# Kernel tuning notes

Hardware: AMD Instinct MI355X
Metric: run time of the kernel (lower is better)

Reference implementation:

```python
import jax, jax.numpy as jnp
import numpy as np

B, S, D, H, FF = 2, 2048, 1024, 16, 4096
HD = D // H          # head dim = 64
ROT = HD // 2        # rotary dim = dim/(num_heads*2) = 32 (partial rotation)
EPS = 1e-5


def setup_inputs() -> dict:
    key = jax.random.key(0)
    ks = jax.random.split(key, 16)
    std = 0.02
    return {
        "x": jax.random.normal(ks[0], (B, S, D), jnp.float32),
        "mask": jnp.ones((B, 1, 1, S), jnp.int32),
        "wq": jax.random.normal(ks[1], (D, D), jnp.float32) * std,
        "bq": jnp.zeros((D,), jnp.float32),
        "wk": jax.random.normal(ks[2], (D, D), jnp.float32) * std,
        "bk": jnp.zeros((D,), jnp.float32),
        "wv": jax.random.normal(ks[3], (D, D), jnp.float32) * std,
        "bv": jnp.zeros((D,), jnp.float32),
        "wo": jax.random.normal(ks[4], (D, D), jnp.float32) * std,
        "bo": jnp.zeros((D,), jnp.float32),
        "ln1_w": jnp.ones((D,), jnp.float32),
        "ln1_b": jnp.zeros((D,), jnp.float32),
        "ln2_w": jnp.ones((D,), jnp.float32),
        "ln2_b": jnp.zeros((D,), jnp.float32),
        "w1": jax.random.normal(ks[5], (D, FF), jnp.float32) * std,
        "b1": jnp.zeros((FF,), jnp.float32),
        "w2": jax.random.normal(ks[6], (FF, D), jnp.float32) * std,
        "b2": jnp.zeros((D,), jnp.float32),
    }


def _layernorm(x, w, b):
    mu = jnp.mean(x, axis=-1, keepdims=True)
    var = jnp.mean(jnp.square(x - mu), axis=-1, keepdims=True)
    return (x - mu) * jax.lax.rsqrt(var + EPS) * w + b


def _rope(t):
    # t: [B, H, S, HD]; rotate first ROT features, interleaved (GPT-J) pairing
    inv_freq = 1.0 / (10000.0 ** (jnp.arange(0, ROT, 2, dtype=jnp.float32) / ROT))
    ang = jnp.arange(S, dtype=jnp.float32)[:, None] * inv_freq      # [S, ROT//2]
    ang = jnp.repeat(ang, 2, axis=-1)                               # [S, ROT]
    cos, sin = jnp.cos(ang), jnp.sin(ang)
    t_rot, t_pass = t[..., :ROT], t[..., ROT:]
    pr = t_rot.reshape(*t_rot.shape[:-1], ROT // 2, 2)
    rot = jnp.stack([-pr[..., 1], pr[..., 0]], axis=-1).reshape(t_rot.shape)
    return jnp.concatenate([t_rot * cos + rot * sin, t_pass], axis=-1)


def reference(x, mask, wq, bq, wk, bk, wv, bv, wo, bo,
              ln1_w, ln1_b, ln2_w, ln2_b, w1, b1, w2, b2):
    res = x
    h = _layernorm(x, ln1_w, ln1_b)
    q = (h @ wq + bq).reshape(B, S, H, HD).transpose(0, 2, 1, 3)
    k = (h @ wk + bk).reshape(B, S, H, HD).transpose(0, 2, 1, 3)
    v = (h @ wv + bv).reshape(B, S, H, HD).transpose(0, 2, 1, 3)
    q, k = _rope(q), _rope(k)
    score = jnp.einsum('bhqd,bhkd->bhqk', q, k) * (1.0 / np.sqrt(HD))
    score = jnp.where(mask == 0, jnp.float32(-1e9), score)
    attn = jax.nn.softmax(score, axis=-1)
    out = jnp.einsum('bhqk,bhkd->bhqd', attn, v)
    out = out.transpose(0, 2, 1, 3).reshape(B, S, D) @ wo + bo
    x = res + out
    res = x
    h = _layernorm(x, ln2_w, ln2_b)
    h = jax.nn.gelu(h @ w1 + b1, approximate=False) @ w2 + b2
    return res + h
```

## Files before the change

### kernel.cpp

```cpp
#include <hip/hip_runtime.h>
#include <cstdint>
#include <cstddef>


typedef __bf16 bf16;
typedef __bf16 bf16x2 __attribute__((ext_vector_type(2)));
typedef __bf16 bf16x4v __attribute__((ext_vector_type(4)));
typedef __bf16 bf16x8 __attribute__((ext_vector_type(8)));
typedef float  f32x4  __attribute__((ext_vector_type(4)));

#define NB 2
#define NS 2048
#define ND 1024
#define NH 16
#define NHD 64
#define NFF 4096
#define NM (NB*NS)
#define QKSCALE 0.18033688011112042f

typedef uint32_t __attribute__((address_space(1))) gu32_t;
typedef uint32_t __attribute__((address_space(3))) lu32_t;
__device__ __forceinline__ void async_copy16(void* lds, const void* g) {
  __builtin_amdgcn_global_load_lds((gu32_t*)g, (lu32_t*)lds, 16, 0, 0);
}

__device__ __forceinline__ float gelu_f(float x) {
  return 0.5f * x * (1.0f + erff(x * 0.70710678118654752f));
}

__global__ __launch_bounds__(256) void prep_kernel(
    const float* __restrict__ wq, const float* __restrict__ wk,
    const float* __restrict__ wv, const float* __restrict__ wo,
    const float* __restrict__ w1, const float* __restrict__ w2,
    bf16* __restrict__ wqt, bf16* __restrict__ wkt, bf16* __restrict__ wvt,
    bf16* __restrict__ wot, bf16* __restrict__ w1t, bf16* __restrict__ w2t,
    const float* __restrict__ bq, const float* __restrict__ bk,
    const float* __restrict__ bv, float* __restrict__ bcat,
    const int* __restrict__ mask, float* __restrict__ m01f,
    bf16* __restrict__ m01b, float2* __restrict__ rtab,
    const float* __restrict__ x, const float* __restrict__ ln1w,
    const float* __restrict__ ln1b, bf16* __restrict__ h1) {
  int flat = blockIdx.x;
  int t = threadIdx.x;
  if (flat < 12288) {
    __shared__ float tile[32][33];
    const float* W; bf16* Wt; long bx, by; int K, N;
    if (flat < 4096) {
      int which = flat >> 10, r = flat & 1023;
      const float* Ws[4] = {wq, wk, wv, wo};
      bf16* Wts[4] = {wqt, wkt, wvt, wot};
      W = Ws[which]; Wt = Wts[which]; bx = r & 31; by = r >> 5; K = ND; N = ND;
    } else if (flat < 8192) {
      int r = flat - 4096;
      W = w1; Wt = w1t; bx = r & 127; by = r >> 7; K = ND; N = NFF;
    } else {
      int r = flat - 8192;
      W = w2; Wt = w2t; bx = r & 31; by = r >> 5; K = NFF; N = ND;
    }
    int tx = t & 31, ty = t >> 5;
#pragma unroll
    for (int r = 0; r < 4; ++r)
      tile[ty + r*8][tx] = W[(by*32 + ty + r*8) * (long)N + bx*32 + tx];
    __syncthreads();
#pragma unroll
    for (int r = 0; r < 4; ++r)
      Wt[(bx*32 + ty + r*8) * (long)K + by*32 + tx] = (bf16)tile[tx][ty + r*8];
  } else if (flat < 12444) {
    int blk = flat - 12288;
    if (blk < 12) {
      int i = blk * 256 + t;
      bcat[i] = (i < ND) ? bq[i] : ((i < 2*ND) ? bk[i - ND] : bv[i - 2*ND]);
    } else if (blk < 28) {
      int i = (blk - 12) * 256 + t;
      float v = mask[i] ? 1.0f : 0.0f;
      m01f[i] = v;
      m01b[i] = (bf16)v;
    } else {
      int idx = (blk - 28) * 256 + t;
      int s = idx >> 4, i = idx & 15;
      float ang = (float)s * exp2f(-(float)i * (13.287712379549449f / 16.0f));
      float sn, cs;
      sincosf(ang, &sn, &cs);
      rtab[idx] = make_float2(cs, sn);
    }
  } else {
    long row = flat - 12444;
    float4 v = ((const float4*)(x + row*ND))[t];
    float s  = v.x + v.y + v.z + v.w;
    float sq = v.x*v.x + v.y*v.y + v.z*v.z + v.w*v.w;
#pragma unroll
    for (int m = 1; m <= 32; m <<= 1) { s += __shfl_xor(s, m); sq += __shfl_xor(sq, m); }
    __shared__ float ss[4], ssq[4];
    if ((t & 63) == 0) { ss[t>>6] = s; ssq[t>>6] = sq; }
    __syncthreads();
    s  = ss[0] + ss[1] + ss[2] + ss[3];
    sq = ssq[0] + ssq[1] + ssq[2] + ssq[3];
    float mu = s * (1.0f/ND);
    float rs = rsqrtf(sq * (1.0f/ND) - mu*mu + 1e-5f);
    float4 wv4 = ((const float4*)ln1w)[t];
    float4 bv4 = ((const float4*)ln1b)[t];
    bf16x4v o;
    o[0] = (bf16)((v.x-mu)*rs*wv4.x + bv4.x);
    o[1] = (bf16)((v.y-mu)*rs*wv4.y + bv4.y);
    o[2] = (bf16)((v.z-mu)*rs*wv4.z + bv4.z);
    o[3] = (bf16)((v.w-mu)*rs*wv4.w + bv4.w);
    *(bf16x4v*)(h1 + row*ND + t*4) = o;
  }
}

__global__ __launch_bounds__(256) void vtrans_kernel(
    const bf16* __restrict__ v, bf16* __restrict__ vt) {
  __shared__ bf16 t[64][66];
  int st = blockIdx.x, bh = blockIdx.y;
  int b = bh >> 4, h = bh & 15;
  int c = threadIdx.x & 63, rg = threadIdx.x >> 6;
  const bf16* src = v + ((long)b*NS + st*64)*ND + h*64;
#pragma unroll
  for (int i = 0; i < 16; ++i) {
    int r = rg*16 + i;
    t[r][c] = src[(long)r*ND + c];
  }
  __syncthreads();
  bf16* dst = vt + (long)bh*64*NS + st*64;
#pragma unroll
  for (int i = 0; i < 16; ++i) {
    int d = rg*16 + i;
    dst[(long)d*NS + c] = t[c][d];
  }
}

__global__ __launch_bounds__(256) void ln_kernel(
    const float* __restrict__ x, const float* __restrict__ w,
    const float* __restrict__ b, bf16* __restrict__ out) {
  long row = blockIdx.x;
  int t = threadIdx.x;
  float4 v = ((const float4*)(x + row*ND))[t];
  float s  = v.x + v.y + v.z + v.w;
  float sq = v.x*v.x + v.y*v.y + v.z*v.z + v.w*v.w;
#pragma unroll
  for (int m = 1; m <= 32; m <<= 1) { s += __shfl_xor(s, m); sq += __shfl_xor(sq, m); }
  __shared__ float ss[4], ssq[4];
  if ((t & 63) == 0) { ss[t>>6] = s; ssq[t>>6] = sq; }
  __syncthreads();
  s  = ss[0] + ss[1] + ss[2] + ss[3];
  sq = ssq[0] + ssq[1] + ssq[2] + ssq[3];
  float mu = s * (1.0f/ND);
  float rs = rsqrtf(sq * (1.0f/ND) - mu*mu + 1e-5f);
  float4 wv = ((const float4*)w)[t];
  float4 bv = ((const float4*)b)[t];
  bf16x4v o;
  o[0] = (bf16)((v.x-mu)*rs*wv.x + bv.x);
  o[1] = (bf16)((v.y-mu)*rs*wv.y + bv.y);
  o[2] = (bf16)((v.z-mu)*rs*wv.z + bv.z);
  o[3] = (bf16)((v.w-mu)*rs*wv.w + bv.w);
  *(bf16x4v*)(out + row*ND + t*4) = o;
}

__global__ __launch_bounds__(256) void ffn2red_kernel(
    const bf16* __restrict__ P, const float* __restrict__ y1,
    const float* __restrict__ b2, float* __restrict__ out) {
  const long n8 = (long)NM * ND / 8;
  for (long i = (long)blockIdx.x*256 + threadIdx.x; i < n8;
       i += (long)gridDim.x*256) {
    bf16x8 p0 = ((const bf16x8*)P)[i];
    bf16x8 p1 = ((const bf16x8*)P)[i + n8];
    bf16x8 p2 = ((const bf16x8*)P)[i + 2*n8];
    bf16x8 p3 = ((const bf16x8*)P)[i + 3*n8];
    float4 ya = ((const float4*)y1)[2*i];
    float4 yb = ((const float4*)y1)[2*i + 1];
    int cb = (int)((i * 8) & 1023);
    float4 ba = *(const float4*)&b2[cb];
    float4 bb = *(const float4*)&b2[cb + 4];
    float4 ra, rb;
    ra.x = ((float)p0[0]+(float)p1[0])+((float)p2[0]+(float)p3[0]) + ya.x + ba.x;
    ra.y = ((float)p0[1]+(float)p1[1])+((float)p2[1]+(float)p3[1]) + ya.y + ba.y;
    ra.z = ((float)p0[2]+(float)p1[2])+((float)p2[2]+(float)p3[2]) + ya.z + ba.z;
    ra.w = ((float)p0[3]+(float)p1[3])+((float)p2[3]+(float)p3[3]) + ya.w + ba.w;
    rb.x = ((float)p0[4]+(float)p1[4])+((float)p2[4]+(float)p3[4]) + yb.x + bb.x;
    rb.y = ((float)p0[5]+(float)p1[5])+((float)p2[5]+(float)p3[5]) + yb.y + bb.y;
    rb.z = ((float)p0[6]+(float)p1[6])+((float)p2[6]+(float)p3[6]) + yb.z + bb.z;
    rb.w = ((float)p0[7]+(float)p1[7])+((float)p2[7]+(float)p3[7]) + yb.w + bb.w;
    ((float4*)out)[2*i]     = ra;
    ((float4*)out)[2*i + 1] = rb;
  }
}

template<int EPI>
__global__ __launch_bounds__(512, 2) void gemm256_kernel(
    const bf16* __restrict__ A, const bf16* __restrict__ Bt,
    const float* __restrict__ bias, void* __restrict__ Cout,
    const float2* __restrict__ rtab, const float* __restrict__ m01f,
    int M, int N, int K, int lda, int ldbt) {
  __shared__ __align__(16) bf16 Alds[2][256*64];
  __shared__ __align__(16) bf16 Blds[2][256*64];
  const int tid = threadIdx.x, lane = tid & 63, w = tid >> 6;
  const int fr = lane & 15, kg = lane >> 4;
  const int wr = w >> 2, wc = w & 3;
  const int kz = (EPI == 2) ? blockIdx.z : 0;
  const long kofs = (long)kz * K;

  const int gx = gridDim.x;
  int lin = blockIdx.y * gx + blockIdx.x;
  int nwg = gx * gridDim.y;
  int swz = (lin & 7) * (nwg >> 3) + (lin >> 3);
  const long am0 = (long)(swz / gx) * 256;
  const long bn0 = (long)(swz % gx) * 256;

  const f32x4 fzero = {0.f, 0.f, 0.f, 0.f};
  f32x4 acc[8][4];
#pragma unroll
  for (int m = 0; m < 8; ++m)
#pragma unroll
    for (int n = 0; n < 4; ++n) acc[m][n] = fzero;

  auto stage = [&](int kt, int bufi) {
#pragma unroll
    for (int i = 0; i < 4; ++i) {
      int s = i*512 + tid;
      int r = s >> 3, c = (s & 7) ^ (r & 7);
      async_copy16((char*)&Alds[bufi][0] + i*8192 + w*1024,
                   &A[(am0 + r)*(long)lda + kofs + kt + c*8]);
    }
#pragma unroll
    for (int i = 0; i < 4; ++i) {
      int s = i*512 + tid;
      int r = s >> 3, c = (s & 7) ^ (r & 7);
      async_copy16((char*)&Blds[bufi][0] + i*8192 + w*1024,
                   &Bt[(bn0 + r)*(long)ldbt + kofs + kt + c*8]);
    }
  };

  const int nk = K >> 6;
  stage(0, 0);
  stage(64, 1);
  asm volatile("s_waitcnt vmcnt(8)" ::: "memory");
  __builtin_amdgcn_s_barrier();
  __builtin_amdgcn_sched_barrier(0);

  for (int t = 0; t < nk; ++t) {
    const char* Ab = (const char*)&Alds[t & 1][0];
    const char* Bb = (const char*)&Blds[t & 1][0];
    bf16x8 bfv0[4], bfv1[4], af[4];
#pragma unroll
    for (int n = 0; n < 4; ++n) {
      int r = wc*64 + n*16 + fr;
      bfv0[n] = *(const bf16x8*)(Bb + r*128 + ((kg ^ (r & 7)) << 4));
    }
#pragma unroll
    for (int m = 0; m < 4; ++m) {
      int r = wr*128 + m*16 + fr;
      af[m] = *(const bf16x8*)(Ab + r*128 + ((kg ^ (r & 7)) << 4));
    }
    asm volatile("s_waitcnt lgkmcnt(0)" ::: "memory");
    __builtin_amdgcn_sched_barrier(0);
    __builtin_amdgcn_s_setprio(1);
#pragma unroll
    for (int m = 0; m < 4; ++m)
#pragma unroll
      for (int n = 0; n < 4; ++n)
        acc[m][n] = __builtin_amdgcn_mfma_f32_16x16x32_bf16(af[m], bfv0[n], acc[m][n], 0, 0, 0);
    __builtin_amdgcn_s_setprio(0);
#pragma unroll
    for (int n = 0; n < 4; ++n) {
      int r = wc*64 + n*16 + fr;
      bfv1[n] = *(const bf16x8*)(Bb + r*128 + (((4 + kg) ^ (r & 7)) << 4));
    }
#pragma unroll
    for (int m = 0; m < 4; ++m) {
      int r = wr*128 + m*16 + fr;
      af[m] = *(const bf16x8*)(Ab + r*128 + (((4 + kg) ^ (r & 7)) << 4));
    }
    asm volatile("s_waitcnt lgkmcnt(0)" ::: "memory");
    __builtin_amdgcn_sched_barrier(0);
    __builtin_amdgcn_s_setprio(1);
#pragma unroll
    for (int m = 0; m < 4; ++m)
#pragma unroll
      for (int n = 0; n < 4; ++n)
        acc[m][n] = __builtin_amdgcn_mfma_f32_16x16x32_bf16(af[m], bfv1[n], acc[m][n], 0, 0, 0);
    __builtin_amdgcn_s_setprio(0);
#pragma unroll
    for (int m = 0; m < 4; ++m) {
      int r = wr*128 + (m+4)*16 + fr;
      af[m] = *(const bf16x8*)(Ab + r*128 + ((kg ^ (r & 7)) << 4));
    }
    asm volatile("s_waitcnt lgkmcnt(0)" ::: "memory");
    __builtin_amdgcn_sched_barrier(0);
    __builtin_amdgcn_s_setprio(1);
#pragma unroll
    for (int m = 0; m < 4; ++m)
#pragma unroll
      for (int n = 0; n < 4; ++n)
        acc[m+4][n] = __builtin_amdgcn_mfma_f32_16x16x32_bf16(af[m], bfv0[n], acc[m+4][n], 0, 0, 0);
    __builtin_amdgcn_s_setprio(0);
#pragma unroll
    for (int m = 0; m < 4; ++m) {
      int r = wr*128 + (m+4)*16 + fr;
      af[m] = *(const bf16x8*)(Ab + r*128 + (((4 + kg) ^ (r & 7)) << 4));
    }
    asm volatile("s_waitcnt lgkmcnt(0)" ::: "memory");
    __builtin_amdgcn_sched_barrier(0);
    __builtin_amdgcn_s_setprio(1);
#pragma unroll
    for (int m = 0; m < 4; ++m)
#pragma unroll
      for (int n = 0; n < 4; ++n)
        acc[m+4][n] = __builtin_amdgcn_mfma_f32_16x16x32_bf16(af[m], bfv1[n], acc[m+4][n], 0, 0, 0);
    __builtin_amdgcn_s_setprio(0);

    if (t + 1 == nk) break;
    __builtin_amdgcn_s_barrier();
    __builtin_amdgcn_sched_barrier(0);
    if (t + 2 < nk) {
      stage((t + 2) * 64, t & 1);
      asm volatile("s_waitcnt vmcnt(8)" ::: "memory");
    } else {
      asm volatile("s_waitcnt vmcnt(0)" ::: "memory");
    }
    __builtin_amdgcn_s_barrier();
    __builtin_amdgcn_sched_barrier(0);
  }

  const int rbase = kg * 4;
  const int region = (int)(bn0 >> 10);
#pragma unroll
  for (int m = 0; m < 8; ++m) {
#pragma unroll
    for (int n = 0; n < 4; ++n) {
      long col = bn0 + wc*64 + n*16 + fr;
      float bia = (EPI == 2) ? 0.0f : bias[col];
#pragma unroll
      for (int j = 0; j < 4; ++j) {
        long row = am0 + wr*128 + m*16 + rbase + j;
        float val = acc[m][n][j] + bia;
        if (EPI == 1) {
          ((bf16*)Cout)[row * N + col] = (bf16)gelu_f(val);
        } else if (EPI == 2) {
          ((bf16*)Cout)[((long)kz * NM + row) * N + col] = (bf16)val;
        } else {
          long cv = col & 1023;
          if (region <= 1) {
            float pval = __shfl_xor(val, 1);
            if (n < 2) {
              float2 cs = rtab[((row & (NS-1)) << 4) | ((n*16 + fr) >> 1)];
              val = (fr & 1) ? val*cs.x + pval*cs.y : val*cs.x - pval*cs.y;
            }
            if (region == 0) val *= QKSCALE;
          } else {
            val *= m01f[row];
          }
          ((bf16*)Cout)[(long)region * (NM*(long)ND) + row * ND + cv] = (bf16)val;
        }
      }
    }
  }
}

__global__ __launch_bounds__(512, 1) void gemm128x8_kernel(
    const bf16* __restrict__ A, const bf16* __restrict__ Bt,
    const float* __restrict__ bias, const float* __restrict__ res,
    float* __restrict__ Cout, int M, int N, int K) {
  __shared__ __align__(16) bf16 Alds[4][128*64];
  __shared__ __align__(16) bf16 Blds[4][128*64];
  const int tid = threadIdx.x, lane = tid & 63, w = tid >> 6;
  const int fr = lane & 15, kg = lane >> 4;
  const int wr = w >> 1, wc = w & 1;

  const int gx = gridDim.x;
  int lin = blockIdx.y * gx + blockIdx.x;
  int nwg = gx * gridDim.y;
  int swz = (lin & 7) * (nwg >> 3) + (lin >> 3);
  const long am0 = (long)(swz / gx) * 128;
  const long bn0 = (long)(swz % gx) * 128;

  const f32x4 fzero = {0.f, 0.f, 0.f, 0.f};
  f32x4 acc[2][4];
#pragma unroll
  for (int m = 0; m < 2; ++m)
#pragma unroll
    for (int n = 0; n < 4; ++n) acc[m][n] = fzero;

  auto stage = [&](int kt, int bufi) {
#pragma unroll
    for (int i = 0; i < 2; ++i) {
      int s = i*512 + tid;
      int r = s >> 3, c = (s & 7) ^ (r & 7);
      async_copy16((char*)&Alds[bufi][0] + i*8192 + w*1024,
                   &A[(am0 + r)*K + kt + c*8]);
      async_copy16((char*)&Blds[bufi][0] + i*8192 + w*1024,
                   &Bt[(bn0 + r)*K + kt + c*8]);
    }
  };

  const int nk = K >> 6;
  stage(0, 0);
  stage(64, 1);
  asm volatile("s_waitcnt vmcnt(4)" ::: "memory");
  __builtin_amdgcn_s_barrier();
  __builtin_amdgcn_sched_barrier(0);

  for (int t = 0; t < nk; ++t) {
    const int cur = t & 3;
    if (t + 2 < nk) stage((t + 2) * 64, (t + 2) & 3);
    const char* Ab = (const char*)&Alds[cur][0];
    const char* Bb = (const char*)&Blds[cur][0];
    bf16x8 af[2][2], bfv[2][4];
#pragma unroll
    for (int kk = 0; kk < 2; ++kk) {
#pragma unroll
      for (int m = 0; m < 2; ++m) {
        int r = wr*32 + m*16 + fr;
        af[kk][m] = *(const bf16x8*)(Ab + r*128 + (((kk*4 + kg) ^ (r & 7)) << 4));
      }
#pragma unroll
      for (int n = 0; n < 4; ++n) {
        int r = wc*64 + n*16 + fr;
        bfv[kk][n] = *(const bf16x8*)(Bb + r*128 + (((kk*4 + kg) ^ (r & 7)) << 4));
      }
    }
    asm volatile("s_waitcnt lgkmcnt(0)" ::: "memory");
    __builtin_amdgcn_sched_barrier(0);
    __builtin_amdgcn_s_setprio(1);
#pragma unroll
    for (int kk = 0; kk < 2; ++kk)
#pragma unroll
      for (int m = 0; m < 2; ++m)
#pragma unroll
        for (int n = 0; n < 4; ++n)
          acc[m][n] = __builtin_amdgcn_mfma_f32_16x16x32_bf16(af[kk][m], bfv[kk][n], acc[m][n], 0, 0, 0);
    __builtin_amdgcn_s_setprio(0);
    if (t + 2 < nk) { asm volatile("s_waitcnt vmcnt(4)" ::: "memory"); }
    else            { asm volatile("s_waitcnt vmcnt(0)" ::: "memory"); }
    __builtin_amdgcn_s_barrier();
    __builtin_amdgcn_sched_barrier(0);
  }

  const int rbase = kg * 4;
#pragma unroll
  for (int m = 0; m < 2; ++m) {
#pragma unroll
    for (int n = 0; n < 4; ++n) {
      long col = bn0 + wc*64 + n*16 + fr;
      float bia = bias[col];
#pragma unroll
      for (int j = 0; j < 4; ++j) {
        long row = am0 + wr*32 + m*16 + rbase + j;
        Cout[row * N + col] = acc[m][n][j] + bia + res[row * N + col];
      }
    }
  }
}

__global__ __launch_bounds__(512, 4) void attn_kernel(
    const bf16* __restrict__ q, const bf16* __restrict__ k,
    const bf16* __restrict__ vt, const bf16* __restrict__ m01b,
    bf16* __restrict__ out) {
  int lin = blockIdx.y * 16 + blockIdx.x;
  int swz = (lin & 7) * 64 + (lin >> 3);
  const int qt = swz & 15;
  const int bh = swz >> 4;
  const int b = bh >> 4, h = bh & 15;
  const int tid = threadIdx.x, lane = tid & 63, w = tid >> 6;
  const int fr = lane & 15, kg = lane >> 4;
  const int k8 = kg * 8;
  const int frl = fr & 3, frh = fr >> 2;

  __shared__ __align__(16) bf16 KVlds[4][2][64*64];
  __shared__ __align__(16) bf16 Mlds[NS];

  const long qrow = (long)qt*128 + w*16 + fr;
  const bf16* qbase = q + ((long)b*NS + qrow)*ND + h*NHD;
  bf16x8 qf[2];
  qf[0] = *(const bf16x8*)(qbase + k8);
  qf[1] = *(const bf16x8*)(qbase + 32 + k8);

  const bf16* kbase = k + (long)b*NS*ND + h*NHD;
  const bf16* vtb = vt + (long)bh*64*NS;
  const bf16* mbase = m01b + (long)b*NS;

  if (w < 4) async_copy16((char*)Mlds + w*1024, mbase + tid*8);

  int aK[4][2], aV[2][4];
#pragma unroll
  for (int n = 0; n < 4; ++n) {
    int r = (frh << 3) + ((n & 1) << 2) + frl + ((n >> 1) << 5);
    int swzr = (r & 7) ^ (((r >> 3) & 1) << 2);
#pragma unroll
    for (int kk = 0; kk < 2; ++kk) {
      aK[n][kk] = r*128 + ((((kk << 2) | kg) ^ swzr) << 4);
      asm("" : "+v"(aK[n][kk]));
    }
  }
#pragma unroll
  for (int kk = 0; kk < 2; ++kk)
#pragma unroll
    for (int n2 = 0; n2 < 4; ++n2) {
      int r = n2*16 + fr;
      aV[kk][n2] = r*128 + ((((kk << 2) | kg) ^ (r & 7)) << 4);
      asm("" : "+v"(aV[kk][n2]));
    }

  const int srow = tid >> 3, sc = tid & 7;
  const int csK = (sc ^ (srow & 7) ^ (((srow >> 3) & 1) << 2));
  const int csV = (sc ^ (srow & 7));
  const bf16* kp = kbase + (long)srow*ND + csK*8;
  const bf16* vp = vtb + (long)srow*NS + csV*8;
  const int ldsoff = w*1024;

  const f32x4 fzero = {0.f, 0.f, 0.f, 0.f};
  f32x4 oacc[4], oaccL = fzero;
#pragma unroll
  for (int n = 0; n < 4; ++n) oacc[n] = fzero;

  async_copy16((char*)KVlds + 0*16384 + ldsoff, kp);
  async_copy16((char*)KVlds + 0*16384 + 8192 + ldsoff, vp);
  kp += 64*ND; vp += 64;
  async_copy16((char*)KVlds + 1*16384 + ldsoff, kp);
  async_copy16((char*)KVlds + 1*16384 + 8192 + ldsoff, vp);
  kp += 64*ND; vp += 64;
  asm volatile("s_waitcnt vmcnt(2)" ::: "memory");
  __builtin_amdgcn_s_barrier();
  __builtin_amdgcn_sched_barrier(0);

  const int NT = NS / 64;

#define ATTN_TILE(KT, BUF)                                                     \
  {                                                                            \
    const int kt_ = (KT);                                                      \
    if (kt_ + 2 < NT) {                                                        \
      async_copy16((char*)KVlds + (((BUF)+2)&3)*16384 + ldsoff, kp);           \
      async_copy16((char*)KVlds + (((BUF)+2)&3)*16384 + 8192 + ldsoff, vp);    \
      kp += 64*ND; vp += 64;                                                   \
    }                                                                          \
    bf16x8 vbm0 = *(const bf16x8*)&Mlds[kt_*64 + k8];                          \
    bf16x8 vbm1 = *(const bf16x8*)&Mlds[kt_*64 + 32 + k8];                     \
    f32x4 sacc[4];                                                             \
    _Pragma("unroll")                                                          \
    for (int n = 0; n < 4; ++n) sacc[n] = fzero;                               \
    _Pragma("unroll")                                                          \
    for (int n = 0; n < 4; ++n) {                                              \
      _Pragma("unroll")                                                        \
      for (int kk = 0; kk < 2; ++kk) {                                         \
        bf16x8 kf = *(const bf16x8*)((const char*)KVlds + (BUF)*16384 +        \
                                     aK[n][kk]);                               \
        sacc[n] = __builtin_amdgcn_mfma_f32_16x16x32_bf16(kf, qf[kk],          \
                                                          sacc[n], 0, 0, 0);   \
      }                                                                        \
    }                                                                          \
    float p[4][4];                                                             \
    _Pragma("unroll")                                                          \
    for (int n = 0; n < 4; ++n) {                                              \
      p[n][0] = exp2f(sacc[n][0]);                                             \
      p[n][1] = exp2f(sacc[n][1]);                                             \
      p[n][2] = exp2f(sacc[n][2]);                                             \
      p[n][3] = exp2f(sacc[n][3]);                                             \
    }                                                                          \
    bf16x8 paf[2];                                                             \
    _Pragma("unroll")                                                          \
    for (int n = 0; n < 4; ++n) {                                              \
      _Pragma("unroll")                                                        \
      for (int j = 0; j < 4; ++j)                                              \
        paf[n >> 1][((n & 1) << 2) + j] = (bf16)p[n][j];                       \
    }                                                                          \
    oaccL = __builtin_amdgcn_mfma_f32_16x16x32_bf16(paf[0], vbm0, oaccL,       \
                                                    0, 0, 0);                  \
    oaccL = __builtin_amdgcn_mfma_f32_16x16x32_bf16(paf[1], vbm1, oaccL,       \
                                                    0, 0, 0);                  \
    _Pragma("unroll")                                                          \
    for (int kk = 0; kk < 2; ++kk) {                                           \
      _Pragma("unroll")                                                        \
      for (int n2 = 0; n2 < 4; ++n2) {                                         \
        bf16x8 vb8 = *(const bf16x8*)((const char*)KVlds + (BUF)*16384 +       \
                                      8192 + aV[kk][n2]);                      \
        oacc[n2] = __builtin_amdgcn_mfma_f32_16x16x32_bf16(paf[kk], vb8,       \
                                                           oacc[n2], 0, 0, 0); \
      }                                                                        \
    }                                                                          \
    if (kt_ + 2 < NT)      { asm volatile("s_waitcnt vmcnt(2)" ::: "memory"); }\
    else if (kt_ + 1 < NT) { asm volatile("s_waitcnt vmcnt(0)" ::: "memory"); }\
    __builtin_amdgcn_s_barrier();                                              \
    __builtin_amdgcn_sched_barrier(0);                                         \
  }

  for (int it = 0; it < NT/4; ++it) {
    int kt0 = it * 4;
    ATTN_TILE(kt0 + 0, 0)
    ATTN_TILE(kt0 + 1, 1)
    ATTN_TILE(kt0 + 2, 2)
    ATTN_TILE(kt0 + 3, 3)
  }
#undef ATTN_TILE

#pragma unroll
  for (int j = 0; j < 4; ++j) {
    float inv = 1.0f / oaccL[j];
    long orow = (long)qt*128 + w*16 + kg*4 + j;
    bf16* ob = out + ((long)b*NS + orow)*ND + h*NHD;
#pragma unroll
    for (int n2 = 0; n2 < 4; ++n2) ob[n2*16 + fr] = (bf16)(oacc[n2][j] * inv);
  }
}

extern "C" void kernel_launch(void* const* d_in, const int* in_sizes, int n_in,
                              void* d_out, int out_size, void* d_ws, size_t ws_size,
                              hipStream_t stream) {
  const float* x    = (const float*)d_in[0];
  const int*   mask = (const int*)d_in[1];
  const float* wq   = (const float*)d_in[2];
  const float* bq   = (const float*)d_in[3];
  const float* wk   = (const float*)d_in[4];
  const float* bk   = (const float*)d_in[5];
  const float* wv   = (const float*)d_in[6];
  const float* bv   = (const float*)d_in[7];
  const float* wo   = (const float*)d_in[8];
  const float* bo   = (const float*)d_in[9];
  const float* ln1w = (const float*)d_in[10];
  const float* ln1b = (const float*)d_in[11];
  const float* ln2w = (const float*)d_in[12];
  const float* ln2b = (const float*)d_in[13];
  const float* w1   = (const float*)d_in[14];
  const float* b1   = (const float*)d_in[15];
  const float* w2   = (const float*)d_in[16];
  const float* b2   = (const float*)d_in[17];
  float* out = (float*)d_out;

  char* ws = (char*)d_ws;
  const size_t MB = 1024ull * 1024ull;
  bf16* wqt = (bf16*)(ws + 0*MB);
  bf16* wkt = (bf16*)(ws + 2*MB);
  bf16* wvt = (bf16*)(ws + 4*MB);
  bf16* wot = (bf16*)(ws + 6*MB);
  bf16* w1t = (bf16*)(ws + 8*MB);
  bf16* w2t = (bf16*)(ws + 16*MB);
  bf16* h1   = (bf16*)(ws + 24*MB);
  bf16* qb   = (bf16*)(ws + 32*MB);
  bf16* kb   = (bf16*)(ws + 40*MB);
  bf16* vb   = (bf16*)(ws + 48*MB);
  bf16* vtb  = h1;
  bf16* attnb = (bf16*)(ws + 72*MB);
  bf16* f1   = (bf16*)(ws + 24*MB);
  float* y1  = (float*)(ws + 56*MB);
  bf16* h2   = (bf16*)(ws + 72*MB);
  float* bcat = (float*)(ws + 80*MB);
  float* m01f = (float*)(ws + 80*MB + 16*1024);
  bf16*  m01b = (bf16*) (ws + 80*MB + 32*1024);
  float2* rtab = (float2*)(ws + 80*MB + 48*1024);
  bf16* pK   = (bf16*)(ws + 84*MB);
  const bool use_splitk = (ws_size >= 116ull*MB);
  (void)in_sizes; (void)n_in; (void)out_size;

  prep_kernel<<<16540, 256, 0, stream>>>(wq, wk, wv, wo, w1, w2,
                                         wqt, wkt, wvt, wot, w1t, w2t,
                                         bq, bk, bv, bcat, mask, m01f, m01b,
                                         rtab, x, ln1w, ln1b, h1);

  gemm256_kernel<3><<<dim3(12, 16), 512, 0, stream>>>(h1, wqt, bcat, qb,
                                                      rtab, m01f, NM, 3*ND, ND,
                                                      ND, ND);
  vtrans_kernel<<<dim3(32, 32), 256, 0, stream>>>(vb, vtb);

  attn_kernel<<<dim3(16, 32), 512, 0, stream>>>(qb, kb, vtb, m01b, attnb);

  gemm128x8_kernel<<<dim3(8, 32), 512, 0, stream>>>(attnb, wot, bo, x, y1,
                                                    NM, ND, ND);
  ln_kernel<<<NM, 256, 0, stream>>>(y1, ln2w, ln2b, h2);
  gemm256_kernel<1><<<dim3(16, 16), 512, 0, stream>>>(h2, w1t, b1, f1,
                                                      nullptr, nullptr,
                                                      NM, NFF, ND, ND, ND);
  if (use_splitk) {
    gemm256_kernel<2><<<dim3(4, 16, 4), 512, 0, stream>>>(f1, w2t, nullptr, pK,
                                                          nullptr, nullptr,
                                                          NM, ND, ND, NFF, NFF);
    ffn2red_kernel<<<2048, 256, 0, stream>>>(pK, y1, b2, out);
  } else {
    gemm128x8_kernel<<<dim3(8, 32), 512, 0, stream>>>(f1, w2t, b2, y1, out,
                                                      NM, ND, NFF);
  }
}
```

Before: 262.7 us.

## Software-pipeline attention QK^T one tile ahead with deeper KV prefetch

Restructures the attention inner loop so the QK^T MFMAs for the next KV tile are issued before the exp2/PV work of the current tile, using ping-pong score registers. KV prefetch depth goes from two tiles ahead to three across the four LDS buffers, and s_setprio is raised around the MFMA blocks. The aim is to overlap the exp2 transcendental work and LDS reads with matrix-core work and to hide more global-load latency. The cost is higher register pressure from the extra score accumulators, which could lower occupancy. The wait-count logic also changes and needs the buffer reuse to stay race-free.

```diff
diff --git a/kernel.cpp b/kernel.cpp
--- a/kernel.cpp
+++ b/kernel.cpp
@@ -512,48 +512,66 @@
 #pragma unroll
   for (int n = 0; n < 4; ++n) oacc[n] = fzero;
 
-  async_copy16((char*)KVlds + 0*16384 + ldsoff, kp);
-  async_copy16((char*)KVlds + 0*16384 + 8192 + ldsoff, vp);
-  kp += 64*ND; vp += 64;
-  async_copy16((char*)KVlds + 1*16384 + ldsoff, kp);
-  async_copy16((char*)KVlds + 1*16384 + 8192 + ldsoff, vp);
-  kp += 64*ND; vp += 64;
+#pragma unroll
+  for (int tpre = 0; tpre < 3; ++tpre) {
+    async_copy16((char*)KVlds + tpre*16384 + ldsoff, kp);
+    async_copy16((char*)KVlds + tpre*16384 + 8192 + ldsoff, vp);
+    kp += 64*ND; vp += 64;
+  }
   asm volatile("s_waitcnt vmcnt(2)" ::: "memory");
   __builtin_amdgcn_s_barrier();
   __builtin_amdgcn_sched_barrier(0);
 
   const int NT = NS / 64;
 
-#define ATTN_TILE(KT, BUF)                                                     \
+  f32x4 sA[4], sB[4];
+#pragma unroll
+  for (int n = 0; n < 4; ++n) sA[n] = fzero;
+  __builtin_amdgcn_s_setprio(1);
+#pragma unroll
+  for (int n = 0; n < 4; ++n)
+#pragma unroll
+    for (int kk = 0; kk < 2; ++kk) {
+      bf16x8 kf = *(const bf16x8*)((const char*)KVlds + 0*16384 + aK[n][kk]);
+      sA[n] = __builtin_amdgcn_mfma_f32_16x16x32_bf16(kf, qf[kk], sA[n], 0, 0, 0);
+    }
+  __builtin_amdgcn_s_setprio(0);
+
+#define ATTN_TILE(KT, BUF, SIN, SOUT)                                          \
   {                                                                            \
     const int kt_ = (KT);                                                      \
-    if (kt_ + 2 < NT) {                                                        \
-      async_copy16((char*)KVlds + (((BUF)+2)&3)*16384 + ldsoff, kp);           \
-      async_copy16((char*)KVlds + (((BUF)+2)&3)*16384 + 8192 + ldsoff, vp);    \
+    if (kt_ + 3 < NT) {                                                        \
+      async_copy16((char*)KVlds + (((BUF)+3)&3)*16384 + ldsoff, kp);           \
+      async_copy16((char*)KVlds + (((BUF)+3)&3)*16384 + 8192 + ldsoff, vp);    \
       kp += 64*ND; vp += 64;                                                   \
     }                                                                          \
+                    \
+    if (kt_ + 1 < NT) {                                                        \
+      _Pragma("unroll")                                                        \
+      for (int n = 0; n < 4; ++n) SOUT[n] = fzero;                             \
+      __builtin_amdgcn_s_setprio(1);                                           \
+      _Pragma("unroll")                                                        \
+      for (int n = 0; n < 4; ++n) {                                            \
+        _Pragma("unroll")                                                      \
+        for (int kk = 0; kk < 2; ++kk) {                                       \
+          bf16x8 kf = *(const bf16x8*)((const char*)KVlds +                    \
+                                       (((BUF)+1)&3)*16384 + aK[n][kk]);       \
+          SOUT[n] = __builtin_amdgcn_mfma_f32_16x16x32_bf16(kf, qf[kk],        \
+                                                            SOUT[n], 0, 0, 0); \
+        }                                                                      \
+      }                                                                        \
+      __builtin_amdgcn_s_setprio(0);                                           \
+    }                                                                          \
+                               \
     bf16x8 vbm0 = *(const bf16x8*)&Mlds[kt_*64 + k8];                          \
     bf16x8 vbm1 = *(const bf16x8*)&Mlds[kt_*64 + 32 + k8];                     \
-    f32x4 sacc[4];                                                             \
-    _Pragma("unroll")                                                          \
-    for (int n = 0; n < 4; ++n) sacc[n] = fzero;                               \
-    _Pragma("unroll")                                                          \
-    for (int n = 0; n < 4; ++n) {                                              \
-      _Pragma("unroll")                                                        \
-      for (int kk = 0; kk < 2; ++kk) {                                         \
-        bf16x8 kf = *(const bf16x8*)((const char*)KVlds + (BUF)*16384 +        \
-                                     aK[n][kk]);                               \
-        sacc[n] = __builtin_amdgcn_mfma_f32_16x16x32_bf16(kf, qf[kk],          \
-                                                          sacc[n], 0, 0, 0);   \
-      }                                                                        \
-    }                                                                          \
     float p[4][4];                                                             \
     _Pragma("unroll")                                                          \
     for (int n = 0; n < 4; ++n) {                                              \
-      p[n][0] = exp2f(sacc[n][0]);                                             \
-      p[n][1] = exp2f(sacc[n][1]);                                             \
-      p[n][2] = exp2f(sacc[n][2]);                                             \
-      p[n][3] = exp2f(sacc[n][3]);                                             \
+      p[n][0] = exp2f(SIN[n][0]);                                              \
+      p[n][1] = exp2f(SIN[n][1]);                                              \
+      p[n][2] = exp2f(SIN[n][2]);                                              \
+      p[n][3] = exp2f(SIN[n][3]);                                              \
     }                                                                          \
     bf16x8 paf[2];                                                             \
     _Pragma("unroll")                                                          \
@@ -566,6 +584,7 @@
                                                     0, 0, 0);                  \
     oaccL = __builtin_amdgcn_mfma_f32_16x16x32_bf16(paf[1], vbm1, oaccL,       \
                                                     0, 0, 0);                  \
+    __builtin_amdgcn_s_setprio(1);                                             \
     _Pragma("unroll")                                                          \
     for (int kk = 0; kk < 2; ++kk) {                                           \
       _Pragma("unroll")                                                        \
@@ -576,18 +595,19 @@
                                                            oacc[n2], 0, 0, 0); \
       }                                                                        \
     }                                                                          \
-    if (kt_ + 2 < NT)      { asm volatile("s_waitcnt vmcnt(2)" ::: "memory"); }\
-    else if (kt_ + 1 < NT) { asm volatile("s_waitcnt vmcnt(0)" ::: "memory"); }\
+    __builtin_amdgcn_s_setprio(0);                                             \
+    if (kt_ + 3 < NT) { asm volatile("s_waitcnt vmcnt(2)" ::: "memory"); }     \
+    else              { asm volatile("s_waitcnt vmcnt(0)" ::: "memory"); }     \
     __builtin_amdgcn_s_barrier();                                              \
     __builtin_amdgcn_sched_barrier(0);                                         \
   }
 
   for (int it = 0; it < NT/4; ++it) {
     int kt0 = it * 4;
-    ATTN_TILE(kt0 + 0, 0)
-    ATTN_TILE(kt0 + 1, 1)
-    ATTN_TILE(kt0 + 2, 2)
-    ATTN_TILE(kt0 + 3, 3)
+    ATTN_TILE(kt0 + 0, 0, sA, sB)
+    ATTN_TILE(kt0 + 1, 1, sB, sA)
+    ATTN_TILE(kt0 + 2, 2, sA, sB)
+    ATTN_TILE(kt0 + 3, 3, sB, sA)
   }
 #undef ATTN_TILE
 
```

Result: no change. 263.8 us (+0.4%).
